# Performance work log

Measured on AMD Instinct MI355X. Metric: run time of the kernel, lower is better.

The kernel has to match this reference:

```python
import jax, jax.numpy as jnp
import numpy as np

ITERATIONS = 10
LAMBDA0 = 0.01


def skew(v):
    # (..., 3) -> (..., 3, 3) skew-symmetric matrices
    x, y, z = v[..., 0], v[..., 1], v[..., 2]
    o = jnp.zeros_like(x)
    return jnp.stack([
        jnp.stack([o, -z, y], -1),
        jnp.stack([z, o, -x], -1),
        jnp.stack([-y, x, o], -1)], -2)


def so3exp_map(w):
    # Rodrigues formula, numerically safe near theta=0
    theta2 = jnp.sum(w * w) + 1e-12
    theta = jnp.sqrt(theta2)
    W = skew(w)
    A = jnp.sin(theta) / theta
    B = (1.0 - jnp.cos(theta)) / theta2
    return jnp.eye(3, dtype=w.dtype) + A * W + B * (W @ W)


def sobel_filter(img):
    # img: (C, H, W) -> (gx, gy) each (C, H, W); depthwise conv, zero pad
    C = img.shape[0]
    kx = jnp.array([[-1., 0., 1.], [-2., 0., 2.], [-1., 0., 1.]], img.dtype)
    k = jnp.stack([kx, kx.T], 0)                       # (2,3,3)
    kern = jnp.broadcast_to(k[None, :, None], (C, 2, 1, 3, 3)).reshape(2 * C, 1, 3, 3)
    out = jax.lax.conv_general_dilated(img[None], kern, (1, 1), 'SAME',
                                       feature_group_count=C)[0]
    return out[0::2], out[1::2]


def from_homogeneous(x):
    return x[..., :-1] / x[..., -1:]


def _forward(q_matrix, r_matrix, points_2d, points_3d, query_feat, reference_feat, K1, size_ratio):
    C, H, W = query_feat.shape
    rel = q_matrix @ jnp.linalg.inv(r_matrix)
    R = rel[:3, :3]
    t = rel[3, :3]  # faithful to original (bottom row)
    gx, gy = sobel_filter(query_feat)

    idx0 = jnp.floor(points_2d / size_ratio).astype(jnp.int32)
    ix0 = jnp.clip(idx0[:, 0], 0, W - 1)
    iy0 = jnp.clip(idx0[:, 1], 0, H - 1)
    feat0 = reference_feat[:, iy0, ix0].T              # (N, C)

    pts_h = jnp.concatenate([points_3d, jnp.ones_like(points_3d[:, :1])], -1)
    pts0 = from_homogeneous(pts_h @ r_matrix.T)        # (N, 3)

    fx, fy = K1[0, 0], K1[1, 1]
    N = pts0.shape[0]
    I3 = jnp.broadcast_to(jnp.eye(3, dtype=pts0.dtype), (N, 3, 3))

    def gather_idx(p2d):
        ii = jnp.floor(p2d / size_ratio).astype(jnp.int32)
        return jnp.clip(ii[:, 0], 0, W - 1), jnp.clip(ii[:, 1], 0, H - 1)

    def step(carry, i):
        R, t, lam, prev = carry
        pts1 = pts0 @ R + t                            # (N, 3) (faithful: R, not R.T)
        ix, iy = gather_idx(from_homogeneous(pts1 @ K1.T))
        err = query_feat[:, iy, ix].T - feat0          # (N, C)
        cost = jnp.sum(err * err, -1)                  # squared_loss, weights = 1
        prev = jnp.where(i == 0, cost.mean(), prev)

        J_p_T = jnp.concatenate([I3, -skew(pts1)], -1)  # (N, 3, 6)
        x, y, z = pts1[:, 0], pts1[:, 1], pts1[:, 2]
        o, zz = jnp.ones_like(x), jnp.zeros_like(x)
        J_h_p = jnp.stack([o * fx, zz, -fx * x / z,
                           zz, o * fy, -fy * y / z], -1).reshape(N, 2, 3)
        J_h_p = J_h_p / z[:, None, None] / size_ratio   # (N, 2, 3)
        gxf = gx[:, iy, ix].T
        gyf = gy[:, iy, ix].T
        J_e_h = jnp.stack([gxf, gyf], -1)               # (N, C, 2)
        J = jnp.einsum('ncu,nuk->nck', J_e_h, J_h_p @ J_p_T)  # (N, C, 6)

        g = jnp.einsum('nck,nc->k', J, err)             # (6,)
        Hs = jnp.einsum('nck,ncl->kl', J, J)            # (6, 6)
        D = jnp.diag(jnp.diag(Hs) + 1e-9)
        delta = -(jnp.linalg.inv(Hs + D * lam) @ g)

        dt, dw = delta[:3], delta[3:6]
        dr = so3exp_map(dw)
        R_new = dr @ R
        t_new = dr @ t + dt
        npts = pts0 @ R_new.T + t_new
        jx, jy = gather_idx(from_homogeneous(npts @ K1.T))
        nerr = query_feat[:, jy, jx].T - feat0
        ncost = jnp.sum(nerr * nerr, -1).mean()

        bad = jnp.isnan(ncost) | jnp.any(jnp.isnan(delta))
        worse = ncost > prev
        lam_upd = jnp.clip(lam * jnp.where(worse, 10., 0.1), 1e-6, 100.)
        lam = jnp.where(bad, lam, lam_upd)
        accept = jnp.logical_not(worse | bad)
        R = jnp.where(accept, R_new, R)
        t = jnp.where(accept, t_new, t)
        prev = jnp.where(accept, ncost, prev)
        return (R, t, lam, prev), None

    lam0 = jnp.asarray(LAMBDA0, pts0.dtype)
    prev0 = jnp.asarray(jnp.inf, pts0.dtype)
    (R, t, _, _), _ = jax.lax.scan(step, (R, t, lam0, prev0), jnp.arange(ITERATIONS))
    return R, t


def setup_inputs() -> dict:
    key = jax.random.key(0)
    k1, k2, k3, k4, k5 = jax.random.split(key, 5)
    N, C, H, W = 8192, 1024, 128, 128
    size_ratio = 8
    f, cx, cy = 1200.0, 512.0, 512.0
    K1 = jnp.array([[f, 0., cx], [0., f, cy], [0., 0., 1.]], jnp.float32)
    # 3D points whose identity-pose projection lands inside the 1024px image
    uv = jax.random.uniform(k1, (N, 2), jnp.float32, 100.0, 900.0)
    z = jax.random.uniform(k2, (N, 1), jnp.float32, 4.0, 8.0)
    points_3d = jnp.concatenate([(uv - jnp.array([cx, cy])) / f * z, z], -1)
    points_2d = jax.random.uniform(k3, (N, 2), jnp.float32, 0.0, 1023.0)
    query_feat = jax.random.normal(k4, (C, H, W), jnp.float32) * 0.1
    reference_feat = jax.random.normal(k5, (C, H, W), jnp.float32) * 0.1
    return {
        'q_matrix': jnp.eye(4, dtype=jnp.float32),
        'r_matrix': jnp.eye(4, dtype=jnp.float32),
        'points_2d': points_2d,
        'points_3d': points_3d,
        'query_feat': query_feat,
        'reference_feat': reference_feat,
        'K1': K1,
        'size_ratio': size_ratio,
    }


def reference(q_matrix, r_matrix, points_2d, points_3d, query_feat, reference_feat, K1, size_ratio):
    return _forward(q_matrix, r_matrix, points_2d, points_3d, query_feat,
                    reference_feat, K1, size_ratio)
```

## Files before the change

kernel.cpp:

```cpp
#include <hip/hip_runtime.h>
#include <math.h>

constexpr int C_  = 1024;
constexpr int H_  = 128;
constexpr int W_  = 128;
constexpr int HW_ = H_ * W_;
constexpr int N_  = 8192;
constexpr int NCOMP = 28;
constexpr int ITERS = 10;
constexpr int NB_ = 2048;


__global__ void k_setup(const float* __restrict__ q, const float* __restrict__ r,
                        const float* __restrict__ K1, const int* __restrict__ srp,
                        const float* __restrict__ p3d, const float* __restrict__ p2d,
                        float* __restrict__ st, float* __restrict__ pts0,
                        int* __restrict__ pix0) {
    int n = blockIdx.x * blockDim.x + threadIdx.x;
    if (n < N_) {
        float sr = (float)srp[0];
        float ph[4] = { p3d[n*3+0], p3d[n*3+1], p3d[n*3+2], 1.f };
        float h[4];
        for (int i = 0; i < 4; i++) {
            float s = 0.f;
            for (int j = 0; j < 4; j++) s += r[i*4+j] * ph[j];
            h[i] = s;
        }
        pts0[n*3+0] = h[0]/h[3];
        pts0[n*3+1] = h[1]/h[3];
        pts0[n*3+2] = h[2]/h[3];
        int ix = (int)floorf(p2d[n*2+0] / sr); ix = min(max(ix, 0), W_-1);
        int iy = (int)floorf(p2d[n*2+1] / sr); iy = min(max(iy, 0), H_-1);
        pix0[n] = iy * W_ + ix;
    }
    if (blockIdx.x == 0 && threadIdx.x == 0) {
        double a[4][8];
        for (int i = 0; i < 4; i++)
            for (int j = 0; j < 4; j++) { a[i][j] = r[i*4+j]; a[i][j+4] = (i == j) ? 1.0 : 0.0; }
        for (int col = 0; col < 4; col++) {
            int piv = col; double mx = fabs(a[col][col]);
            for (int i = col+1; i < 4; i++) if (fabs(a[i][col]) > mx) { mx = fabs(a[i][col]); piv = i; }
            if (piv != col) for (int j = 0; j < 8; j++) { double t = a[col][j]; a[col][j] = a[piv][j]; a[piv][j] = t; }
            double d = a[col][col];
            for (int j = 0; j < 8; j++) a[col][j] /= d;
            for (int i = 0; i < 4; i++) if (i != col) {
                double f = a[i][col];
                for (int j = 0; j < 8; j++) a[i][j] -= f * a[col][j];
            }
        }
        double rel[4][4];
        for (int i = 0; i < 4; i++)
            for (int j = 0; j < 4; j++) {
                double s = 0;
                for (int k = 0; k < 4; k++) s += (double)q[i*4+k] * a[k][j+4];
                rel[i][j] = s;
            }
        for (int i = 0; i < 3; i++)
            for (int j = 0; j < 3; j++) st[i*3+j] = (float)rel[i][j];
        st[9]  = (float)rel[3][0];
        st[10] = (float)rel[3][1];
        st[11] = (float)rel[3][2];
        st[12] = 0.01f;
        st[13] = __builtin_inff();
        for (int i = 0; i < 9; i++) st[32+i] = K1[i];
        st[41] = K1[0]; st[42] = K1[4];
        st[43] = (float)srp[0];
    }
}

template <bool SOBEL>
__global__ void k_transpose2(const float* __restrict__ src, float* __restrict__ dq,
                             float* __restrict__ dgx, float* __restrict__ dgy) {
    constexpr int CT = 16, YT = 4, XT = 32;
    constexpr int RS = YT + 2;
    constexpr int CS = XT + 2;
    constexpr int PCS = 35;
    constexpr int CHS = RS * PCS + 1;
    __shared__ float lds[CT * CHS];
    const int x0 = blockIdx.x * XT;
    const int y0 = blockIdx.y * YT;
    const int cc = blockIdx.z * CT;
    const int tid = threadIdx.x;
    for (int idx = tid; idx < CT * RS * CS; idx += 256) {
        int c   = idx / (RS * CS);
        int rem = idx % (RS * CS);
        int r   = rem / CS;
        int x   = rem % CS;
        int gy  = y0 + r - 1;
        int gx  = x0 + x - 1;
        float v = 0.f;
        if (gy >= 0 && gy < H_ && gx >= 0 && gx < W_)
            v = src[(size_t)(cc + c) * HW_ + gy * W_ + gx];
        lds[c * CHS + r * PCS + x] = v;
    }
    __syncthreads();
    const int c       = tid & 15;
    const int s       = tid >> 4;
    const int row     = s >> 2;
    const int colbase = (s & 3) * 8;
    const float* Lt = &lds[c * CHS + row * PCS + colbase];
    const float* Lm = Lt + PCS;
    const float* Lb = Lm + PCS;
    size_t o = ((size_t)((y0 + row) * W_ + x0 + colbase)) * C_ + cc + c;
    if (!SOBEL) {
        for (int cx = 0; cx < 8; cx++, o += C_)
            dq[o] = Lm[cx + 1];
    } else {
        float t0l = Lt[0], t0m = Lt[1];
        float t1l = Lm[0], t1m = Lm[1];
        float t2l = Lb[0], t2m = Lb[1];
        for (int cx = 0; cx < 8; cx++, o += C_) {
            float t0r = Lt[cx + 2];
            float t1r = Lm[cx + 2];
            float t2r = Lb[cx + 2];
            dq[o]  = t1m;
            dgx[o] = (t0r - t0l) + 2.f*(t1r - t1l) + (t2r - t2l);
            dgy[o] = (t2l + 2.f*t2m + t2r) - (t0l + 2.f*t0m + t0r);
            t0l = t0m; t0m = t0r;
            t1l = t1m; t1m = t1r;
            t2l = t2m; t2m = t2r;
        }
    }
}

__global__ __launch_bounds__(256) void k_feat0(const float* __restrict__ rT,
                                               const int* __restrict__ pix0,
                                               float* __restrict__ feat0) {
    const int w = threadIdx.x >> 6, lane = threadIdx.x & 63;
    const int n = blockIdx.x * 4 + w;
    const float4* s = (const float4*)(rT + (size_t)pix0[n] * C_);
    float4* d = (float4*)(feat0 + (size_t)n * C_);
#pragma unroll
    for (int i = 0; i < 4; i++) d[i*64 + lane] = s[i*64 + lane];
}

__device__ inline float sel6(int k, float v0, float v1, float v2,
                             float v3, float v4, float v5) {
    return k==0 ? v0 : k==1 ? v1 : k==2 ? v2 : k==3 ? v3 : k==4 ? v4 : v5;
}

__global__ __launch_bounds__(256) void k_passA(const float* __restrict__ qT,
        const float* __restrict__ gxT, const float* __restrict__ gyT,
        const float* __restrict__ feat0, const float* __restrict__ pts0,
        const float* __restrict__ st, float* __restrict__ partial) {
    const int w = threadIdx.x >> 6, lane = threadIdx.x & 63;
    const int n = blockIdx.x * 4 + w;
    const float p0 = pts0[n*3+0], p1 = pts0[n*3+1], p2 = pts0[n*3+2];
    const float X = p0*st[0] + p1*st[3] + p2*st[6] + st[9];
    const float Y = p0*st[1] + p1*st[4] + p2*st[7] + st[10];
    const float Z = p0*st[2] + p1*st[5] + p2*st[8] + st[11];
    const float hx = st[32]*X + st[33]*Y + st[34]*Z;
    const float hy = st[35]*X + st[36]*Y + st[37]*Z;
    const float hz = st[38]*X + st[39]*Y + st[40]*Z;
    const float sr = st[43];
    const float u = hx / hz, v = hy / hz;
    int ix = (int)floorf(u / sr); ix = min(max(ix, 0), W_-1);
    int iy = (int)floorf(v / sr); iy = min(max(iy, 0), H_-1);
    const int pix = iy * W_ + ix;

    const float4* q4 = (const float4*)(qT  + (size_t)pix * C_);
    const float4* g4 = (const float4*)(gxT + (size_t)pix * C_);
    const float4* h4 = (const float4*)(gyT + (size_t)pix * C_);
    const float4* f4 = (const float4*)(feat0 + (size_t)n * C_);

    float cost = 0, bx = 0, by = 0, mxx = 0, mxy = 0, myy = 0;
#pragma unroll
    for (int i = 0; i < 4; i++) {
        float4 qv = q4[i*64 + lane], gv = g4[i*64 + lane];
        float4 yv = h4[i*64 + lane], fv = f4[i*64 + lane];
        float e;
        e = qv.x - fv.x; cost += e*e; bx += gv.x*e; by += yv.x*e; mxx += gv.x*gv.x; mxy += gv.x*yv.x; myy += yv.x*yv.x;
        e = qv.y - fv.y; cost += e*e; bx += gv.y*e; by += yv.y*e; mxx += gv.y*gv.y; mxy += gv.y*yv.y; myy += yv.y*yv.y;
        e = qv.z - fv.z; cost += e*e; bx += gv.z*e; by += yv.z*e; mxx += gv.z*gv.z; mxy += gv.z*yv.z; myy += yv.z*yv.z;
        e = qv.w - fv.w; cost += e*e; bx += gv.w*e; by += yv.w*e; mxx += gv.w*gv.w; mxy += gv.w*yv.w; myy += yv.w*yv.w;
    }
#pragma unroll
    for (int off = 32; off; off >>= 1) {
        cost += __shfl_xor(cost, off, 64);
        bx   += __shfl_xor(bx,   off, 64);
        by   += __shfl_xor(by,   off, 64);
        mxx  += __shfl_xor(mxx,  off, 64);
        mxy  += __shfl_xor(mxy,  off, 64);
        myy  += __shfl_xor(myy,  off, 64);
    }

    const float fx = st[41], fy = st[42];
    const float sc = 1.f / (Z * sr);
    const float jh00 = fx, jh02 = -fx * X / Z;
    const float jh11 = fy, jh12 = -fy * Y / Z;
    const float a00 = sc*jh00, a01 = 0.f,     a02 = sc*jh02;
    const float a03 = sc*(jh02*Y), a04 = sc*(jh00*Z - jh02*X), a05 = sc*(-jh00*Y);
    const float a10 = 0.f,     a11 = sc*jh11, a12 = sc*jh12;
    const float a13 = sc*(-jh11*Z + jh12*Y), a14 = sc*(-jh12*X), a15 = sc*(jh11*X);

    float val = 0.f;
    const int t = lane;
    if (t == 0) {
        val = cost;
    } else if (t < 7) {
        int k = t - 1;
        val = sel6(k,a00,a01,a02,a03,a04,a05)*bx + sel6(k,a10,a11,a12,a13,a14,a15)*by;
    } else if (t < NCOMP) {
        int idx = t - 7, k = 0;
        while (idx >= 6 - k) { idx -= 6 - k; k++; }
        int l = k + idx;
        float A0k = sel6(k,a00,a01,a02,a03,a04,a05);
        float A1k = sel6(k,a10,a11,a12,a13,a14,a15);
        float A0l = sel6(l,a00,a01,a02,a03,a04,a05);
        float A1l = sel6(l,a10,a11,a12,a13,a14,a15);
        val = A0k*A0l*mxx + (A0k*A1l + A1k*A0l)*mxy + A1k*A1l*myy;
    }

    __shared__ float pl[4][NCOMP];
    if (t < NCOMP) pl[w][t] = val;
    __syncthreads();
    if (threadIdx.x < NCOMP)
        partial[(size_t)threadIdx.x * NB_ + blockIdx.x] =
            pl[0][threadIdx.x] + pl[1][threadIdx.x] + pl[2][threadIdx.x] + pl[3][threadIdx.x];
}

__global__ void k_RS(const float* __restrict__ partial, float* __restrict__ st,
                     int iter) {
    const int tid = threadIdx.x;
    const int w = tid >> 6, lane = tid & 63;
    for (int comp = w; comp < NCOMP; comp += 16) {
        double s = 0;
#pragma unroll 4
        for (int i = 0; i < NB_/64; i++)
            s += (double)partial[(size_t)comp * NB_ + i*64 + lane];
        for (int off = 32; off; off >>= 1) s += __shfl_down(s, off, 64);
        if (lane == 0) st[44 + comp] = (float)s;
    }
    __syncthreads();
    if (tid != 0) return;

    double costsum = st[44];
    if (iter == 0) st[13] = (float)(costsum / (double)N_);
    double g[6];
    for (int k = 0; k < 6; k++) g[k] = st[45+k];
    double Hs[6][6];
    int idx = 51;
    for (int k = 0; k < 6; k++)
        for (int l = k; l < 6; l++) { Hs[k][l] = st[idx]; Hs[l][k] = st[idx]; idx++; }
    double lam = st[12];
    double M[6][7];
    for (int i = 0; i < 6; i++) {
        for (int j = 0; j < 6; j++) M[i][j] = Hs[i][j];
        M[i][i] += (Hs[i][i] + 1e-9) * lam;
        M[i][6] = -g[i];
    }
    for (int col = 0; col < 6; col++) {
        int piv = col; double mx = fabs(M[col][col]);
        for (int i = col+1; i < 6; i++) if (fabs(M[i][col]) > mx) { mx = fabs(M[i][col]); piv = i; }
        if (piv != col) for (int j = col; j < 7; j++) { double t = M[col][j]; M[col][j] = M[piv][j]; M[piv][j] = t; }
        double d = M[col][col];
        for (int j = col; j < 7; j++) M[col][j] /= d;
        for (int i = 0; i < 6; i++) if (i != col) {
            double f = M[i][col];
            if (f != 0.0) for (int j = col; j < 7; j++) M[i][j] -= f * M[col][j];
        }
    }
    double delta[6];
    int bad = 0;
    for (int i = 0; i < 6; i++) {
        delta[i] = M[i][6];
        st[26+i] = (float)delta[i];
        if (isnan(st[26+i])) bad = 1;
    }
    st[72] = (float)bad;
    double w0 = delta[3], w1 = delta[4], w2 = delta[5];
    double th2 = w0*w0 + w1*w1 + w2*w2 + 1e-12;
    double th = sqrt(th2);
    double Af = sin(th) / th, Bf = (1.0 - cos(th)) / th2;
    double Wm[3][3] = {{0,-w2,w1},{w2,0,-w0},{-w1,w0,0}};
    double W2[3][3];
    for (int i = 0; i < 3; i++)
        for (int j = 0; j < 3; j++) {
            double s2 = 0;
            for (int k = 0; k < 3; k++) s2 += Wm[i][k]*Wm[k][j];
            W2[i][j] = s2;
        }
    double dr[3][3];
    for (int i = 0; i < 3; i++)
        for (int j = 0; j < 3; j++)
            dr[i][j] = (i == j ? 1.0 : 0.0) + Af*Wm[i][j] + Bf*W2[i][j];
    double Rn[3][3];
    for (int i = 0; i < 3; i++)
        for (int j = 0; j < 3; j++) {
            double s2 = 0;
            for (int k = 0; k < 3; k++) s2 += dr[i][k] * (double)st[k*3+j];
            Rn[i][j] = s2;
        }
    for (int i = 0; i < 3; i++)
        for (int j = 0; j < 3; j++) st[14 + i*3 + j] = (float)Rn[i][j];
    for (int i = 0; i < 3; i++) {
        double s2 = 0;
        for (int k = 0; k < 3; k++) s2 += dr[i][k] * (double)st[9+k];
        st[23+i] = (float)(s2 + delta[i]);
    }
}

__global__ __launch_bounds__(256) void k_passB(const float* __restrict__ qT,
        const float* __restrict__ feat0, const float* __restrict__ pts0,
        const float* __restrict__ st, float* __restrict__ ncostp) {
    const int w = threadIdx.x >> 6, lane = threadIdx.x & 63;
    const int n = blockIdx.x * 4 + w;
    const float p0 = pts0[n*3+0], p1 = pts0[n*3+1], p2 = pts0[n*3+2];
    const float X = p0*st[14] + p1*st[15] + p2*st[16] + st[23];
    const float Y = p0*st[17] + p1*st[18] + p2*st[19] + st[24];
    const float Z = p0*st[20] + p1*st[21] + p2*st[22] + st[25];
    const float hx = st[32]*X + st[33]*Y + st[34]*Z;
    const float hy = st[35]*X + st[36]*Y + st[37]*Z;
    const float hz = st[38]*X + st[39]*Y + st[40]*Z;
    const float sr = st[43];
    const float u = hx / hz, v = hy / hz;
    int ix = (int)floorf(u / sr); ix = min(max(ix, 0), W_-1);
    int iy = (int)floorf(v / sr); iy = min(max(iy, 0), H_-1);
    const int pix = iy * W_ + ix;

    const float4* q4 = (const float4*)(qT + (size_t)pix * C_);
    const float4* f4 = (const float4*)(feat0 + (size_t)n * C_);
    float cost = 0;
#pragma unroll
    for (int i = 0; i < 4; i++) {
        float4 qv = q4[i*64 + lane], fv = f4[i*64 + lane];
        float e;
        e = qv.x - fv.x; cost += e*e;
        e = qv.y - fv.y; cost += e*e;
        e = qv.z - fv.z; cost += e*e;
        e = qv.w - fv.w; cost += e*e;
    }
#pragma unroll
    for (int off = 32; off; off >>= 1) cost += __shfl_xor(cost, off, 64);

    __shared__ float pl[4];
    if (lane == 0) pl[w] = cost;
    __syncthreads();
    if (threadIdx.x == 0) ncostp[blockIdx.x] = pl[0] + pl[1] + pl[2] + pl[3];
}

__global__ void k_decide(const float* __restrict__ ncostp, float* __restrict__ st) {
    const int lane = threadIdx.x;
    double s = 0;
#pragma unroll 4
    for (int i = 0; i < NB_/64; i++) s += (double)ncostp[i*64 + lane];
    for (int off = 32; off; off >>= 1) s += __shfl_down(s, off, 64);
    if (lane == 0) {
        float nc = (float)(s / (double)N_);
        float prev = st[13], lam = st[12];
        bool bad = isnan(nc) || (st[72] != 0.f);
        bool worse = nc > prev;
        float lu = lam * (worse ? 10.f : 0.1f);
        lu = fminf(fmaxf(lu, 1e-6f), 100.f);
        st[12] = bad ? lam : lu;
        bool accept = !(worse || bad);
        if (accept) {
            for (int i = 0; i < 9; i++) st[i] = st[14+i];
            for (int i = 0; i < 3; i++) st[9+i] = st[23+i];
            st[13] = nc;
        }
    }
}

__global__ void k_out(const float* __restrict__ st, float* __restrict__ out) {
    int i = threadIdx.x;
    if (i < 12) out[i] = st[i];
}

extern "C" void kernel_launch(void* const* d_in, const int* in_sizes, int n_in,
                              void* d_out, int out_size, void* d_ws, size_t ws_size,
                              hipStream_t stream) {
    const float* q   = (const float*)d_in[0];
    const float* r   = (const float*)d_in[1];
    const float* p2d = (const float*)d_in[2];
    const float* p3d = (const float*)d_in[3];
    const float* qf  = (const float*)d_in[4];
    const float* rf  = (const float*)d_in[5];
    const float* K1  = (const float*)d_in[6];
    const int*   srp = (const int*)d_in[7];

    float* ws = (float*)d_ws;
    size_t off = 0;
    float* qT    = ws + off; off += (size_t)HW_ * C_;
    float* gxT   = ws + off; off += (size_t)HW_ * C_;
    float* gyT   = ws + off; off += (size_t)HW_ * C_;
    float* feat0 = ws + off; off += (size_t)N_ * C_;
    float* pts0  = ws + off; off += 3 * N_;
    int*   pix0  = (int*)(ws + off); off += N_;
    float* partial = ws + off; off += (size_t)NCOMP * NB_;
    float* ncostp  = ws + off; off += NB_;
    float* st    = ws + off; off += 128;

    k_setup<<<N_/256, 256, 0, stream>>>(q, r, K1, srp, p3d, p2d, st, pts0, pix0);
    k_transpose2<false><<<dim3(W_/32, H_/4, C_/16), 256, 0, stream>>>(rf, qT, nullptr, nullptr);
    k_feat0<<<NB_, 256, 0, stream>>>(qT, pix0, feat0);
    k_transpose2<true><<<dim3(W_/32, H_/4, C_/16), 256, 0, stream>>>(qf, qT, gxT, gyT);

    for (int it = 0; it < ITERS; it++) {
        k_passA<<<NB_, 256, 0, stream>>>(qT, gxT, gyT, feat0, pts0, st, partial);
        k_RS<<<1, 1024, 0, stream>>>(partial, st, it);
        k_passB<<<NB_, 256, 0, stream>>>(qT, feat0, pts0, st, ncostp);
        k_decide<<<1, 64, 0, stream>>>(ncostp, st);
    }
    k_out<<<1, 64, 0, stream>>>(st, (float*)d_out);
}
```

Measured before the change: 851.8 us.

## Fuse reductions into passes via last-block atomics, interleave q/gx/gy, gather feat0 directly

```diff
diff --git a/kernel.cpp b/kernel.cpp
--- a/kernel.cpp
+++ b/kernel.cpp
@@ -9,13 +9,14 @@
 constexpr int NCOMP = 28;
 constexpr int ITERS = 10;
 constexpr int NB_ = 2048;
+constexpr int ROWF = 3 * C_;
 
 
 __global__ void k_setup(const float* __restrict__ q, const float* __restrict__ r,
                         const float* __restrict__ K1, const int* __restrict__ srp,
                         const float* __restrict__ p3d, const float* __restrict__ p2d,
                         float* __restrict__ st, float* __restrict__ pts0,
-                        int* __restrict__ pix0) {
+                        int* __restrict__ pix0, int* __restrict__ cnt) {
     int n = blockIdx.x * blockDim.x + threadIdx.x;
     if (n < N_) {
         float sr = (float)srp[0];
@@ -33,6 +34,7 @@
         int iy = (int)floorf(p2d[n*2+1] / sr); iy = min(max(iy, 0), H_-1);
         pix0[n] = iy * W_ + ix;
     }
+    if (blockIdx.x == 0 && threadIdx.x < 32) cnt[threadIdx.x] = 0;
     if (blockIdx.x == 0 && threadIdx.x == 0) {
         double a[4][8];
         for (int i = 0; i < 4; i++)
@@ -65,13 +67,12 @@
         for (int i = 0; i < 9; i++) st[32+i] = K1[i];
         st[41] = K1[0]; st[42] = K1[4];
         st[43] = (float)srp[0];
-    }
-}
-
-template <bool SOBEL>
-__global__ void k_transpose2(const float* __restrict__ src, float* __restrict__ dq,
-                             float* __restrict__ dgx, float* __restrict__ dgy) {
-    constexpr int CT = 16, YT = 4, XT = 32;
+        st[72] = 0.f;
+    }
+}
+
+__global__ void k_sobelT(const float* __restrict__ src, float* __restrict__ qgg) {
+    constexpr int CT = 32, YT = 4, XT = 32;
     constexpr int RS = YT + 2;
     constexpr int CS = XT + 2;
     constexpr int PCS = 35;
@@ -94,44 +95,43 @@
         lds[c * CHS + r * PCS + x] = v;
     }
     __syncthreads();
-    const int c       = tid & 15;
-    const int s       = tid >> 4;
-    const int row     = s >> 2;
-    const int colbase = (s & 3) * 8;
-    const float* Lt = &lds[c * CHS + row * PCS + colbase];
+    const int c    = tid & 31;
+    const int slot = tid >> 5;
+    const int row  = slot >> 1;
+    const int xh   = (slot & 1) * 16;
+    const float* Lt = &lds[c * CHS + row * PCS + xh];
     const float* Lm = Lt + PCS;
     const float* Lb = Lm + PCS;
-    size_t o = ((size_t)((y0 + row) * W_ + x0 + colbase)) * C_ + cc + c;
-    if (!SOBEL) {
-        for (int cx = 0; cx < 8; cx++, o += C_)
-            dq[o] = Lm[cx + 1];
-    } else {
-        float t0l = Lt[0], t0m = Lt[1];
-        float t1l = Lm[0], t1m = Lm[1];
-        float t2l = Lb[0], t2m = Lb[1];
-        for (int cx = 0; cx < 8; cx++, o += C_) {
-            float t0r = Lt[cx + 2];
-            float t1r = Lm[cx + 2];
-            float t2r = Lb[cx + 2];
-            dq[o]  = t1m;
-            dgx[o] = (t0r - t0l) + 2.f*(t1r - t1l) + (t2r - t2l);
-            dgy[o] = (t2l + 2.f*t2m + t2r) - (t0l + 2.f*t0m + t0r);
-            t0l = t0m; t0m = t0r;
-            t1l = t1m; t1m = t1r;
-            t2l = t2m; t2m = t2r;
-        }
-    }
-}
-
-__global__ __launch_bounds__(256) void k_feat0(const float* __restrict__ rT,
-                                               const int* __restrict__ pix0,
-                                               float* __restrict__ feat0) {
+    size_t o = ((size_t)((y0 + row) * W_ + x0 + xh)) * ROWF + cc + c;
+    float t0l = Lt[0], t0m = Lt[1];
+    float t1l = Lm[0], t1m = Lm[1];
+    float t2l = Lb[0], t2m = Lb[1];
+    for (int cx = 0; cx < 16; cx++, o += ROWF) {
+        float t0r = Lt[cx + 2];
+        float t1r = Lm[cx + 2];
+        float t2r = Lb[cx + 2];
+        qgg[o]          = t1m;
+        qgg[o + C_]     = (t0r - t0l) + 2.f*(t1r - t1l) + (t2r - t2l);
+        qgg[o + 2*C_]   = (t2l + 2.f*t2m + t2r) - (t0l + 2.f*t0m + t0r);
+        t0l = t0m; t0m = t0r;
+        t1l = t1m; t1m = t1r;
+        t2l = t2m; t2m = t2r;
+    }
+}
+
+__global__ __launch_bounds__(256) void k_feat0d(const float* __restrict__ rf,
+                                                const int* __restrict__ pix0,
+                                                float* __restrict__ feat0) {
     const int w = threadIdx.x >> 6, lane = threadIdx.x & 63;
     const int n = blockIdx.x * 4 + w;
-    const float4* s = (const float4*)(rT + (size_t)pix0[n] * C_);
-    float4* d = (float4*)(feat0 + (size_t)n * C_);
+    const int p = pix0[n];
+    const float* base = rf + p;
+    float* dst = feat0 + (size_t)n * C_;
 #pragma unroll
-    for (int i = 0; i < 4; i++) d[i*64 + lane] = s[i*64 + lane];
+    for (int i = 0; i < 16; i++) {
+        int c = lane + 64 * i;
+        dst[c] = base[(size_t)c * HW_];
+    }
 }
 
 __device__ inline float sel6(int k, float v0, float v1, float v2,
@@ -139,10 +139,10 @@
     return k==0 ? v0 : k==1 ? v1 : k==2 ? v2 : k==3 ? v3 : k==4 ? v4 : v5;
 }
 
-__global__ __launch_bounds__(256) void k_passA(const float* __restrict__ qT,
-        const float* __restrict__ gxT, const float* __restrict__ gyT,
+__global__ __launch_bounds__(256, 4) void k_passA(const float* __restrict__ qgg,
         const float* __restrict__ feat0, const float* __restrict__ pts0,
-        const float* __restrict__ st, float* __restrict__ partial) {
+        float* __restrict__ st, float* __restrict__ partial,
+        int* __restrict__ cnt, int iter) {
     const int w = threadIdx.x >> 6, lane = threadIdx.x & 63;
     const int n = blockIdx.x * 4 + w;
     const float p0 = pts0[n*3+0], p1 = pts0[n*3+1], p2 = pts0[n*3+2];
@@ -158,16 +158,16 @@
     int iy = (int)floorf(v / sr); iy = min(max(iy, 0), H_-1);
     const int pix = iy * W_ + ix;
 
-    const float4* q4 = (const float4*)(qT  + (size_t)pix * C_);
-    const float4* g4 = (const float4*)(gxT + (size_t)pix * C_);
-    const float4* h4 = (const float4*)(gyT + (size_t)pix * C_);
-    const float4* f4 = (const float4*)(feat0 + (size_t)n * C_);
+    const float4* row4 = (const float4*)(qgg + (size_t)pix * ROWF);
+    const float4* f4   = (const float4*)(feat0 + (size_t)n * C_);
 
     float cost = 0, bx = 0, by = 0, mxx = 0, mxy = 0, myy = 0;
 #pragma unroll
     for (int i = 0; i < 4; i++) {
-        float4 qv = q4[i*64 + lane], gv = g4[i*64 + lane];
-        float4 yv = h4[i*64 + lane], fv = f4[i*64 + lane];
+        float4 qv = row4[      lane + 64*i];
+        float4 gv = row4[256 + lane + 64*i];
+        float4 yv = row4[512 + lane + 64*i];
+        float4 fv = f4[lane + 64*i];
         float e;
         e = qv.x - fv.x; cost += e*e; bx += gv.x*e; by += yv.x*e; mxx += gv.x*gv.x; mxy += gv.x*yv.x; myy += yv.x*yv.x;
         e = qv.y - fv.y; cost += e*e; bx += gv.y*e; by += yv.y*e; mxx += gv.y*gv.y; mxy += gv.y*yv.y; myy += yv.y*yv.y;
@@ -212,36 +212,43 @@
     }
 
     __shared__ float pl[4][NCOMP];
+    __shared__ int lastFlag;
     if (t < NCOMP) pl[w][t] = val;
     __syncthreads();
     if (threadIdx.x < NCOMP)
-        partial[(size_t)threadIdx.x * NB_ + blockIdx.x] =
-            pl[0][threadIdx.x] + pl[1][threadIdx.x] + pl[2][threadIdx.x] + pl[3][threadIdx.x];
-}
-
-__global__ void k_RS(const float* __restrict__ partial, float* __restrict__ st,
-                     int iter) {
-    const int tid = threadIdx.x;
-    const int w = tid >> 6, lane = tid & 63;
-    for (int comp = w; comp < NCOMP; comp += 16) {
+        __hip_atomic_store(&partial[(size_t)threadIdx.x * NB_ + blockIdx.x],
+                           pl[0][threadIdx.x] + pl[1][threadIdx.x] +
+                           pl[2][threadIdx.x] + pl[3][threadIdx.x],
+                           __ATOMIC_RELAXED, __HIP_MEMORY_SCOPE_AGENT);
+    __syncthreads();
+    if (threadIdx.x == 0) {
+        int old = __hip_atomic_fetch_add(&cnt[iter], 1, __ATOMIC_RELAXED,
+                                         __HIP_MEMORY_SCOPE_AGENT);
+        lastFlag = (old == NB_ - 1);
+    }
+    __syncthreads();
+    if (!lastFlag) return;
+
+    __shared__ double sred[NCOMP];
+    for (int j = 0; j < 7; j++) {
+        int comp = w + 4 * j;
         double s = 0;
-#pragma unroll 4
         for (int i = 0; i < NB_/64; i++)
-            s += (double)partial[(size_t)comp * NB_ + i*64 + lane];
+            s += (double)__hip_atomic_load(&partial[(size_t)comp * NB_ + i*64 + lane],
+                                           __ATOMIC_RELAXED, __HIP_MEMORY_SCOPE_AGENT);
         for (int off = 32; off; off >>= 1) s += __shfl_down(s, off, 64);
-        if (lane == 0) st[44 + comp] = (float)s;
-    }
-    __syncthreads();
-    if (tid != 0) return;
-
-    double costsum = st[44];
-    if (iter == 0) st[13] = (float)(costsum / (double)N_);
+        if (lane == 0) sred[comp] = s;
+    }
+    __syncthreads();
+    if (threadIdx.x != 0) return;
+
+    if (iter == 0) st[13] = (float)(sred[0] / (double)N_);
     double g[6];
-    for (int k = 0; k < 6; k++) g[k] = st[45+k];
+    for (int k = 0; k < 6; k++) g[k] = sred[1+k];
     double Hs[6][6];
-    int idx = 51;
+    int idx = 7;
     for (int k = 0; k < 6; k++)
-        for (int l = k; l < 6; l++) { Hs[k][l] = st[idx]; Hs[l][k] = st[idx]; idx++; }
+        for (int l = k; l < 6; l++) { Hs[k][l] = sred[idx]; Hs[l][k] = sred[idx]; idx++; }
     double lam = st[12];
     double M[6][7];
     for (int i = 0; i < 6; i++) {
@@ -252,7 +259,7 @@
     for (int col = 0; col < 6; col++) {
         int piv = col; double mx = fabs(M[col][col]);
         for (int i = col+1; i < 6; i++) if (fabs(M[i][col]) > mx) { mx = fabs(M[i][col]); piv = i; }
-        if (piv != col) for (int j = col; j < 7; j++) { double t = M[col][j]; M[col][j] = M[piv][j]; M[piv][j] = t; }
+        if (piv != col) for (int j = col; j < 7; j++) { double tt = M[col][j]; M[col][j] = M[piv][j]; M[piv][j] = tt; }
         double d = M[col][col];
         for (int j = col; j < 7; j++) M[col][j] /= d;
         for (int i = 0; i < 6; i++) if (i != col) {
@@ -300,9 +307,10 @@
     }
 }
 
-__global__ __launch_bounds__(256) void k_passB(const float* __restrict__ qT,
+__global__ __launch_bounds__(256, 4) void k_passB(const float* __restrict__ qgg,
         const float* __restrict__ feat0, const float* __restrict__ pts0,
-        const float* __restrict__ st, float* __restrict__ ncostp) {
+        float* __restrict__ st, float* __restrict__ ncostp,
+        int* __restrict__ cnt, int iter, float* __restrict__ out) {
     const int w = threadIdx.x >> 6, lane = threadIdx.x & 63;
     const int n = blockIdx.x * 4 + w;
     const float p0 = pts0[n*3+0], p1 = pts0[n*3+1], p2 = pts0[n*3+2];
@@ -318,12 +326,12 @@
     int iy = (int)floorf(v / sr); iy = min(max(iy, 0), H_-1);
     const int pix = iy * W_ + ix;
 
-    const float4* q4 = (const float4*)(qT + (size_t)pix * C_);
-    const float4* f4 = (const float4*)(feat0 + (size_t)n * C_);
+    const float4* row4 = (const float4*)(qgg + (size_t)pix * ROWF);
+    const float4* f4   = (const float4*)(feat0 + (size_t)n * C_);
     float cost = 0;
 #pragma unroll
     for (int i = 0; i < 4; i++) {
-        float4 qv = q4[i*64 + lane], fv = f4[i*64 + lane];
+        float4 qv = row4[lane + 64*i], fv = f4[lane + 64*i];
         float e;
         e = qv.x - fv.x; cost += e*e;
         e = qv.y - fv.y; cost += e*e;
@@ -334,16 +342,27 @@
     for (int off = 32; off; off >>= 1) cost += __shfl_xor(cost, off, 64);
 
     __shared__ float pl[4];
+    __shared__ int lastFlag;
     if (lane == 0) pl[w] = cost;
     __syncthreads();
-    if (threadIdx.x == 0) ncostp[blockIdx.x] = pl[0] + pl[1] + pl[2] + pl[3];
-}
-
-__global__ void k_decide(const float* __restrict__ ncostp, float* __restrict__ st) {
-    const int lane = threadIdx.x;
+    if (threadIdx.x == 0)
+        __hip_atomic_store(&ncostp[blockIdx.x], pl[0] + pl[1] + pl[2] + pl[3],
+                           __ATOMIC_RELAXED, __HIP_MEMORY_SCOPE_AGENT);
+    __syncthreads();
+    if (threadIdx.x == 0) {
+        int old = __hip_atomic_fetch_add(&cnt[16 + iter], 1, __ATOMIC_RELAXED,
+                                         __HIP_MEMORY_SCOPE_AGENT);
+        lastFlag = (old == NB_ - 1);
+    }
+    __syncthreads();
+    if (!lastFlag) return;
+
+    if (threadIdx.x >= 64) return;
     double s = 0;
 #pragma unroll 4
-    for (int i = 0; i < NB_/64; i++) s += (double)ncostp[i*64 + lane];
+    for (int i = 0; i < NB_/64; i++)
+        s += (double)__hip_atomic_load(&ncostp[i*64 + lane],
+                                       __ATOMIC_RELAXED, __HIP_MEMORY_SCOPE_AGENT);
     for (int off = 32; off; off >>= 1) s += __shfl_down(s, off, 64);
     if (lane == 0) {
         float nc = (float)(s / (double)N_);
@@ -359,12 +378,9 @@
             for (int i = 0; i < 3; i++) st[9+i] = st[23+i];
             st[13] = nc;
         }
-    }
-}
-
-__global__ void k_out(const float* __restrict__ st, float* __restrict__ out) {
-    int i = threadIdx.x;
-    if (i < 12) out[i] = st[i];
+        if (iter == ITERS - 1)
+            for (int i = 0; i < 12; i++) out[i] = st[i];
+    }
 }
 
 extern "C" void kernel_launch(void* const* d_in, const int* in_sizes, int n_in,
@@ -381,26 +397,21 @@
 
     float* ws = (float*)d_ws;
     size_t off = 0;
-    float* qT    = ws + off; off += (size_t)HW_ * C_;
-    float* gxT   = ws + off; off += (size_t)HW_ * C_;
-    float* gyT   = ws + off; off += (size_t)HW_ * C_;
+    float* qgg   = ws + off; off += (size_t)HW_ * ROWF;
     float* feat0 = ws + off; off += (size_t)N_ * C_;
     float* pts0  = ws + off; off += 3 * N_;
     int*   pix0  = (int*)(ws + off); off += N_;
     float* partial = ws + off; off += (size_t)NCOMP * NB_;
     float* ncostp  = ws + off; off += NB_;
     float* st    = ws + off; off += 128;
-
-    k_setup<<<N_/256, 256, 0, stream>>>(q, r, K1, srp, p3d, p2d, st, pts0, pix0);
-    k_transpose2<false><<<dim3(W_/32, H_/4, C_/16), 256, 0, stream>>>(rf, qT, nullptr, nullptr);
-    k_feat0<<<NB_, 256, 0, stream>>>(qT, pix0, feat0);
-    k_transpose2<true><<<dim3(W_/32, H_/4, C_/16), 256, 0, stream>>>(qf, qT, gxT, gyT);
+    int*   cnt   = (int*)(ws + off); off += 32;
+
+    k_setup<<<N_/256, 256, 0, stream>>>(q, r, K1, srp, p3d, p2d, st, pts0, pix0, cnt);
+    k_feat0d<<<NB_, 256, 0, stream>>>(rf, pix0, feat0);
+    k_sobelT<<<dim3(W_/32, H_/4, C_/32), 256, 0, stream>>>(qf, qgg);
 
     for (int it = 0; it < ITERS; it++) {
-        k_passA<<<NB_, 256, 0, stream>>>(qT, gxT, gyT, feat0, pts0, st, partial);
-        k_RS<<<1, 1024, 0, stream>>>(partial, st, it);
-        k_passB<<<NB_, 256, 0, stream>>>(qT, feat0, pts0, st, ncostp);
-        k_decide<<<1, 64, 0, stream>>>(ncostp, st);
-    }
-    k_out<<<1, 64, 0, stream>>>(st, (float*)d_out);
-}
+        k_passA<<<NB_, 256, 0, stream>>>(qgg, feat0, pts0, st, partial, cnt, it);
+        k_passB<<<NB_, 256, 0, stream>>>(qgg, feat0, pts0, st, ncostp, cnt, it, (float*)d_out);
+    }
+}
```

Result: slower. 1.195 ms (+40.3%).
